# Performance work log

Hardware: AMD Instinct MI355X
Metric: run time of the kernel (lower is better)

## Reference

```python
import jax, jax.numpy as jnp
import numpy as np

B, T, IN, OUT, H, N, M = 16, 1024, 64, 64, 512, 128, 40
EPS = 1e-8


def setup_inputs() -> dict:
    key = jax.random.key(0)
    ks = jax.random.split(key, 16)
    s = 0.02  # xavier-ish init scale for weights
    inp = {
        "x": jax.random.normal(ks[0], (B, T, IN), jnp.float32),
        "h0": jnp.zeros((B, H), jnp.float32),
        "c0": jnp.zeros((B, H), jnp.float32),
        "memory0": jax.random.normal(ks[1], (B, N, M), jnp.float32) * 0.01,
        "read0": jnp.zeros((B, M), jnp.float32),
        # LSTMCell params (torch gate order: i, f, g, o)
        "W_ih": jax.random.normal(ks[2], (4 * H, IN + M), jnp.float32) * s,
        "b_ih": jnp.zeros((4 * H,), jnp.float32),
        "W_hh": jax.random.normal(ks[3], (4 * H, H), jnp.float32) * s,
        "b_hh": jnp.zeros((4 * H,), jnp.float32),
        "W_fc": jax.random.normal(ks[4], (OUT, H), jnp.float32) * s,
        "b_fc": jnp.zeros((OUT,), jnp.float32),
        "W_e": jax.random.normal(ks[5], (M, H), jnp.float32) * s,
        "b_e": jnp.zeros((M,), jnp.float32),
        "W_a": jax.random.normal(ks[6], (M, H), jnp.float32) * s,
        "b_a": jnp.zeros((M,), jnp.float32),
        "W_k": jax.random.normal(ks[7], (M, H), jnp.float32) * s,
        "b_k": jnp.zeros((M,), jnp.float32),
        "W_b": jax.random.normal(ks[8], (1, H), jnp.float32) * s,
        "b_b": jnp.zeros((1,), jnp.float32),
    }
    return inp


def _ntm_scan(x, h0, c0, memory0, read0, W_ih, b_ih, W_hh, b_hh,
              W_fc, b_fc, W_e, b_e, W_a, b_a, W_k, b_k, W_b, b_b):
    def step(carry, x_t):
        h, c, mem, r = carry
        # controller LSTM cell on [x_t, read_vector]
        inp = jnp.concatenate([x_t, r], axis=-1)            # [B, IN+M]
        gates = inp @ W_ih.T + b_ih + h @ W_hh.T + b_hh      # [B, 4H]
        i, f, g, o = jnp.split(gates, 4, axis=-1)
        i = jax.nn.sigmoid(i); f = jax.nn.sigmoid(f)
        g = jnp.tanh(g);       o = jax.nn.sigmoid(o)
        c = f * c + i * g
        h = o * jnp.tanh(c)
        out = jnp.tanh(h @ W_fc.T + b_fc)                    # [B, OUT]
        # content addressing
        key = jnp.tanh(h @ W_k.T + b_k)                      # [B, M]
        beta = jax.nn.softplus(h @ W_b.T + b_b) + EPS        # [B, 1]
        kn = key / (jnp.linalg.norm(key, axis=-1, keepdims=True) + EPS)
        mn = mem / (jnp.linalg.norm(mem, axis=-1, keepdims=True) + EPS)
        sim = jnp.einsum('bnm,bm->bn', mn, kn)               # [B, N]
        w = jax.nn.softmax(beta * sim, axis=-1)              # [B, N]
        # erase/add write, then read from updated memory
        e = jax.nn.sigmoid(h @ W_e.T + b_e)                  # [B, M]
        a = jnp.tanh(h @ W_a.T + b_a)                        # [B, M]
        mem = mem * (1.0 - w[:, :, None] * e[:, None, :]) + w[:, :, None] * a[:, None, :]
        r = jnp.einsum('bn,bnm->bm', w, mem)                 # [B, M]
        return (h, c, mem, r), out

    xs = jnp.swapaxes(x, 0, 1)                               # [T, B, IN]
    (h, c, mem, r), outs = jax.lax.scan(step, (h0, c0, memory0, read0), xs)
    return jnp.swapaxes(outs, 0, 1), h, c                    # [B, T, OUT]


def reference(x, h0, c0, memory0, read0, W_ih, b_ih, W_hh, b_hh,
              W_fc, b_fc, W_e, b_e, W_a, b_a, W_k, b_k, W_b, b_b):
    return _ntm_scan(x, h0, c0, memory0, read0, W_ih, b_ih, W_hh, b_hh,
                     W_fc, b_fc, W_e, b_e, W_a, b_a, W_k, b_k, W_b, b_b)
```

## Files before the change

### kernel.cpp

```cpp
#include <hip/hip_runtime.h>
#include <math.h>

#define Bq   16
#define Tq   1024
#define OUTq 64
#define Hq   512
#define Nq   128
#define Mq   40
#define NT   512
#define NISL 16
#define GWG  13
#define IWG  14
#define NWG  224
#define EPSq 1e-8f
#define MAGIC 0x00C0FFEEu

typedef unsigned long long ull;

__device__ __forceinline__ float sigmf(float x){ return 1.f/(1.f + expf(-x)); }
__device__ __forceinline__ float softplusf(float x){ return (x > 20.f) ? x : log1pf(expf(x)); }

__device__ __forceinline__ ull icld64(const ull* p){
  return __hip_atomic_load(p, __ATOMIC_RELAXED, __HIP_MEMORY_SCOPE_AGENT);
}
__device__ __forceinline__ void icst64(ull* p, ull v){
  __hip_atomic_store(p, v, __ATOMIC_RELAXED, __HIP_MEMORY_SCOPE_AGENT);
}
__device__ __forceinline__ ull icpoll64(const ull* p){
  ull v;
  asm volatile("global_load_dwordx2 %0, %1, off sc0 sc1\n\ts_waitcnt vmcnt(0)"
               : "=v"(v) : "v"(p) : "memory");
  return v;
}
__device__ __forceinline__ ull packtv(unsigned tag, float v){
  return ((ull)tag << 32) | (ull)__float_as_uint(v);
}
__device__ __forceinline__ float lowf(ull v){ return __uint_as_float((unsigned)v); }

__device__ __forceinline__ float waitword(const ull* sh, unsigned want, bool fast){
  if (fast){
    #pragma unroll 1
    for (int i = 0; i < 4096; ++i){
      const ull v = icpoll64(sh);
      if ((unsigned)(v >> 32) == want) return lowf(v);
      __builtin_amdgcn_s_sleep(1);
    }
  }
  #pragma unroll 1
  for (;;){
    const ull v = icld64(sh);
    if ((unsigned)(v >> 32) == want) return lowf(v);
    __builtin_amdgcn_s_sleep(1);
  }
}

__device__ __forceinline__ int ready_and_handshake(ull* rdy, ull* magic, int blk){
  __hip_atomic_fetch_add(rdy, 1ull, __ATOMIC_RELAXED, __HIP_MEMORY_SCOPE_AGENT);
  while (icld64(rdy) < (ull)NWG) __builtin_amdgcn_s_sleep(8);
  if (blk == 0) icst64(magic, ((ull)MAGIC << 32) | 1ull);
  #pragma unroll 1
  for (int i = 0; i < 4000; ++i){
    if ((unsigned)(icpoll64(magic) >> 32) == MAGIC) return 1;
    __builtin_amdgcn_s_sleep(2);
  }
  return 0;
}

extern "C" __global__ void __launch_bounds__(NT, 1)
ntm_kernel(const float* __restrict__ xg,  const float* __restrict__ h0g,
           const float* __restrict__ c0g, const float* __restrict__ mem0g,
           const float* __restrict__ read0g,
           const float* __restrict__ Wih, const float* __restrict__ bih,
           const float* __restrict__ Whh, const float* __restrict__ bhh,
           const float* __restrict__ Wfc, const float* __restrict__ bfc,
           const float* __restrict__ We,  const float* __restrict__ be,
           const float* __restrict__ Wa,  const float* __restrict__ ba,
           const float* __restrict__ Wk,  const float* __restrict__ bk,
           const float* __restrict__ Wb,  const float* __restrict__ bbeta,
           float* __restrict__ yout, ull* __restrict__ rdy,
           ull* __restrict__ h_sh, ull* __restrict__ r_sh)
{
  const int blk = blockIdx.x;
  const int tid = threadIdx.x;
  const int x   = blk & 7;
  const int j   = blk >> 3;
  const int bat = (j < IWG) ? x : (x + 8);
  const int slot= (j < IWG) ? j : (j - IWG);
  __shared__ __align__(16) char smem[41344];
  __shared__ int s_fast;
  ull* magic = rdy + 1;

  if (slot < GWG){
    float* inp_s  = (float*)smem;
    float* red_s  = (float*)(smem + 2560);
    float* rw_s   = (float*)(smem + 13440);
    float* r_s    = (float*)(smem + 39680);
    float* gate_s = (float*)(smem + 39840);
    float* c_s    = (float*)(smem + 40480);
    float* bias_s = (float*)(smem + 40640);

    const int kseg  = tid & 15;
    const int rslot = tid >> 4;
    const int nd    = (slot < 12) ? 40 : 32;
    const int d0    = slot * 40;
    const int rowsR = 4 * nd;

    float4 w4[5][9];
    #pragma unroll
    for (int rr = 0; rr < 5; ++rr){
      const int row = rslot*5 + rr;
      if (row < rowsR){
        const int gate = row / nd, ld = row - gate*nd;
        const int grow = gate*Hq + d0 + ld;
        #pragma unroll
        for (int kk = 0; kk < 9; ++kk){
          float v[4];
          #pragma unroll
          for (int c4 = 0; c4 < 4; ++c4){
            const int k = kseg*36 + kk*4 + c4;
            v[c4] = (k < 64) ? Wih[grow*104 + k] : Whh[grow*512 + (k - 64)];
          }
          w4[rr][kk] = make_float4(v[0], v[1], v[2], v[3]);
        }
      } else {
        #pragma unroll
        for (int kk = 0; kk < 9; ++kk) w4[rr][kk] = make_float4(0.f,0.f,0.f,0.f);
      }
    }
    if (tid < rowsR){
      const int gate = tid / nd, ld = tid - gate*nd;
      const int grow = gate*Hq + d0 + ld;
      bias_s[tid] = bih[grow] + bhh[grow];
    }
    for (int i = tid; i < rowsR*40; i += NT){
      const int row = i / 40, m = i - row*40;
      const int gate = row / nd, ld = row - gate*nd;
      const int grow = gate*Hq + d0 + ld;
      rw_s[row*41 + m] = Wih[grow*104 + 64 + m];
    }
    if (tid < nd) c_s[tid] = c0g[bat*Hq + d0 + tid];
    if (tid < 16)
      *(float4*)&inp_s[tid*4] = ((const float4*)xg)[(bat*Tq + 0)*16 + tid];
    if (tid < 128)
      *(float4*)&inp_s[64 + tid*4] = ((const float4*)h0g)[bat*128 + tid];
    __syncthreads();
    if (tid == 0) s_fast = ready_and_handshake(rdy, magic, blk);
    __syncthreads();
    const bool fast = (s_fast != 0);

    for (int t = 0; t < Tq; ++t){
      const int p = t & 1, pm = (t - 1) & 1;
      float acc[5] = {0.f,0.f,0.f,0.f,0.f};
      {
        const float* bp = inp_s + kseg*36;
        #pragma unroll
        for (int kk = 0; kk < 9; ++kk){
          const float4 f = *(const float4*)&bp[kk*4];
          #pragma unroll
          for (int rr = 0; rr < 5; ++rr)
            acc[rr] += w4[rr][kk].x*f.x + w4[rr][kk].y*f.y
                     + w4[rr][kk].z*f.z + w4[rr][kk].w*f.w;
        }
      }
      #pragma unroll
      for (int rr = 0; rr < 5; ++rr)
        red_s[(rslot*5 + rr)*17 + kseg] = acc[rr];
      if (t == 0){
        if (tid < 40) r_s[tid] = read0g[bat*Mq + tid];
      } else if (tid < 40){
        const int idx = (pm*NISL + bat)*Mq + tid;
        r_s[tid] = waitword(&r_sh[idx], (unsigned)t, fast);
      }
      __syncthreads();
      if (tid < rowsR){
        float s2 = bias_s[tid];
        const float* rp = &red_s[tid*17];
        #pragma unroll
        for (int q = 0; q < 16; ++q) s2 += rp[q];
        const float* rwp = &rw_s[tid*41];
        #pragma unroll
        for (int m = 0; m < 40; ++m) s2 += rwp[m]*r_s[m];
        gate_s[tid] = s2;
      }
      __syncthreads();
      if (tid < nd){
        const float gi = gate_s[tid];
        const float gf = gate_s[nd + tid];
        const float gc = gate_s[2*nd + tid];
        const float go = gate_s[3*nd + tid];
        const float iv = sigmf(gi), fv = sigmf(gf), gv = tanhf(gc), ov = sigmf(go);
        const float cn = fv*c_s[tid] + iv*gv;
        const float hn = ov*tanhf(cn);
        c_s[tid] = cn;
        const int idx = (p*NISL + bat)*Hq + d0 + tid;
        icst64(&h_sh[idx], packtv((unsigned)(t+1), hn));
        if (t == Tq - 1){
          yout[Bq*Tq*OUTq + bat*Hq + d0 + tid] = hn;
          yout[Bq*Tq*OUTq + Bq*Hq + bat*Hq + d0 + tid] = cn;
        }
      }
      {
        const int idx = (p*NISL + bat)*Hq + tid;
        inp_s[64 + tid] = waitword(&h_sh[idx], (unsigned)(t+1), fast);
      }
      if (t + 1 < Tq && tid < 16)
        *(float4*)&inp_s[tid*4] = ((const float4*)xg)[(bat*Tq + t + 1)*16 + tid];
      __syncthreads();
    }
  }
  else {
    float* mem_s  = (float*)smem;
    float* h_s    = (float*)(smem + 22528);
    float* hred_s = (float*)(smem + 24576);
    float* key_s  = (float*)(smem + 26624);
    float* e_s    = (float*)(smem + 26784);
    float* a_s    = (float*)(smem + 26944);
    float* w_s    = (float*)(smem + 27104);
    float* rred_s = (float*)(smem + 27616);
    float* ored_s = (float*)(smem + 29056);

    #pragma unroll
    for (int q = 0; q < 10; ++q){
      const int e = q*512 + tid;
      const int n = e / 40, m = e - n*40;
      mem_s[n*44 + m] = mem0g[bat*(Nq*Mq) + e];
    }
    const int o  = tid & 127;
    const int kc = tid >> 7;
    const float* wrow = (o < 40) ? (Wk + o*Hq)
                      : (o < 80) ? (We + (o-40)*Hq)
                      : (o < 120) ? (Wa + (o-80)*Hq)
                      : (o == 120) ? Wb : nullptr;
    float4 wv2[32];
    if (wrow){
      #pragma unroll
      for (int kk = 0; kk < 32; ++kk)
        wv2[kk] = *(const float4*)&wrow[kc*128 + kk*4];
    } else {
      #pragma unroll
      for (int kk = 0; kk < 32; ++kk) wv2[kk] = make_float4(0.f,0.f,0.f,0.f);
    }
    float4 wfc[16];
    {
      const int o2 = tid & 63, kc8 = tid >> 6;
      #pragma unroll
      for (int kk = 0; kk < 16; ++kk)
        wfc[kk] = *(const float4*)&Wfc[o2*Hq + kc8*64 + kk*4];
    }
    const float bfcv = bfc[tid & 63];
    float hb0 = 0.f, hb1 = 0.f;
    if (tid < 64){
      const int o0 = tid, o1 = tid + 64;
      hb0 = (o0 < 40) ? bk[o0] : be[o0-40];
      hb1 = (o1 < 80) ? be[o1-40] : (o1 < 120) ? ba[o1-80]
          : (o1 == 120) ? bbeta[0] : 0.f;
    }
    __syncthreads();
    if (tid == 0) s_fast = ready_and_handshake(rdy, magic, blk);
    __syncthreads();
    const bool fast = (s_fast != 0);

    for (int t = 0; t < Tq; ++t){
      const int p = t & 1;
      const unsigned want = (unsigned)(t + 1);
      {
        const int idx = (p*NISL + bat)*Hq + tid;
        h_s[tid] = waitword(&h_sh[idx], want, fast);
      }
      __syncthreads();
      {
        float a0 = 0.f;
        const float* hp = h_s + kc*128;
        #pragma unroll
        for (int kk = 0; kk < 32; ++kk){
          const float4 f = *(const float4*)&hp[kk*4];
          a0 += wv2[kk].x*f.x + wv2[kk].y*f.y + wv2[kk].z*f.z + wv2[kk].w*f.w;
        }
        hred_s[o*4 + kc] = a0;
      }
      __syncthreads();
      if (tid < 64){
        const int l = tid;
        const float4 p0 = *(const float4*)&hred_s[l*4];
        const float4 p1 = *(const float4*)&hred_s[(l+64)*4];
        float s0 = hb0 + p0.x + p0.y + p0.z + p0.w;
        float s1 = hb1 + p1.x + p1.y + p1.z + p1.w;
        float kv = 0.f;
        if (l < 40){ kv = tanhf(s0); key_s[l] = kv; }
        else        { e_s[l-40] = sigmf(s0); }
        if (l < 16)      e_s[l+24]  = sigmf(s1);
        else if (l < 56) a_s[l-16]  = tanhf(s1);
        float bval = softplusf(s1) + EPSq;
        const float bet = __shfl(bval, 56);
        float ss = kv*kv;
        #pragma unroll
        for (int off = 32; off; off >>= 1) ss += __shfl_xor(ss, off);
        const float rinv = 1.f/(sqrtf(ss) + EPSq);
        float sc[2];
        #pragma unroll
        for (int half = 0; half < 2; ++half){
          const int n = l + 64*half;
          float qq = 0.f, dd = 0.f;
          const float* mrow = &mem_s[n*44];
          #pragma unroll
          for (int q = 0; q < 10; ++q){
            const float4 mv = *(const float4*)&mrow[q*4];
            const float4 kvv = *(const float4*)&key_s[q*4];
            qq += mv.x*mv.x + mv.y*mv.y + mv.z*mv.z + mv.w*mv.w;
            dd += mv.x*kvv.x + mv.y*kvv.y + mv.z*kvv.z + mv.w*kvv.w;
          }
          sc[half] = bet * dd * rinv / (sqrtf(qq) + EPSq);
        }
        const float e0 = expf(sc[0]), e1 = expf(sc[1]);
        float sm = e0 + e1;
        #pragma unroll
        for (int off = 32; off; off >>= 1) sm += __shfl_xor(sm, off);
        const float inv = 1.f/sm;
        w_s[l] = e0*inv; w_s[l+64] = e1*inv;
      }
      __syncthreads();
      if (tid < 320){
        const int m = tid % 40, ng = tid / 40;
        const float ev = e_s[m], av = a_s[m];
        float part = 0.f;
        #pragma unroll
        for (int q = 0; q < 16; ++q){
          const int n = ng*16 + q, idx2 = n*44 + m;
          const float mv = mem_s[idx2];
          const float wn = w_s[n];
          const float nv = fmaf(wn, fmaf(-ev, mv, av), mv);
          mem_s[idx2] = nv;
          part = fmaf(wn, nv, part);
        }
        rred_s[m*9 + ng] = part;
      }
      __syncthreads();
      if (tid < 40){
        float r = 0.f;
        #pragma unroll
        for (int q = 0; q < 8; ++q) r += rred_s[tid*9 + q];
        const int idx = (p*NISL + bat)*Mq + tid;
        icst64(&r_sh[idx], packtv(want, r));
      }
      {
        const int o2 = tid & 63, kc8 = tid >> 6;
        float a0 = 0.f;
        const float* hp = h_s + kc8*64;
        #pragma unroll
        for (int kk = 0; kk < 16; ++kk){
          const float4 f = *(const float4*)&hp[kk*4];
          a0 += wfc[kk].x*f.x + wfc[kk].y*f.y + wfc[kk].z*f.z + wfc[kk].w*f.w;
        }
        ored_s[o2*9 + kc8] = a0;
      }
      __syncthreads();
      if (tid < 64){
        float s2 = bfcv;
        const float* op = &ored_s[tid*9];
        #pragma unroll
        for (int q = 0; q < 8; ++q) s2 += op[q];
        yout[(bat*Tq + t)*OUTq + tid] = tanhf(s2);
      }
      __syncthreads();
    }
  }
}

extern "C" void kernel_launch(void* const* d_in, const int* in_sizes, int n_in,
                              void* d_out, int out_size, void* d_ws, size_t ws_size,
                              hipStream_t stream){
  const float* xg    = (const float*)d_in[0];
  const float* h0g   = (const float*)d_in[1];
  const float* c0g   = (const float*)d_in[2];
  const float* mem0g = (const float*)d_in[3];
  const float* read0g= (const float*)d_in[4];
  const float* Wih   = (const float*)d_in[5];
  const float* bih   = (const float*)d_in[6];
  const float* Whh   = (const float*)d_in[7];
  const float* bhh   = (const float*)d_in[8];
  const float* Wfc   = (const float*)d_in[9];
  const float* bfc   = (const float*)d_in[10];
  const float* We    = (const float*)d_in[11];
  const float* be    = (const float*)d_in[12];
  const float* Wa    = (const float*)d_in[13];
  const float* ba    = (const float*)d_in[14];
  const float* Wk    = (const float*)d_in[15];
  const float* bk    = (const float*)d_in[16];
  const float* Wb    = (const float*)d_in[17];
  const float* bbeta = (const float*)d_in[18];

  float* yout  = (float*)d_out;
  ull*   rdy   = (ull*)d_ws;
  ull*   h_sh  = (ull*)((char*)d_ws + 4096);
  ull*   r_sh  = (ull*)((char*)d_ws + 135168);

  hipMemsetAsync(d_ws, 0, 147456, stream);
  hipLaunchKernelGGL(ntm_kernel, dim3(NWG), dim3(NT), 0, stream,
                     xg, h0g, c0g, mem0g, read0g, Wih, bih, Whh, bhh,
                     Wfc, bfc, We, be, Wa, ba, Wk, bk, Wb, bbeta,
                     yout, rdy, h_sh, r_sh);
}
```

Baseline: 6.419 ms.

## Offload head projections of h to gate workgroups and publish partial sums

```diff
diff --git a/kernel.cpp b/kernel.cpp
--- a/kernel.cpp
+++ b/kernel.cpp
@@ -78,7 +78,8 @@
            const float* __restrict__ Wk,  const float* __restrict__ bk,
            const float* __restrict__ Wb,  const float* __restrict__ bbeta,
            float* __restrict__ yout, ull* __restrict__ rdy,
-           ull* __restrict__ h_sh, ull* __restrict__ r_sh)
+           ull* __restrict__ h_sh, ull* __restrict__ r_sh,
+           ull* __restrict__ hp_sh)
 {
   const int blk = blockIdx.x;
   const int tid = threadIdx.x;
@@ -86,7 +87,7 @@
   const int j   = blk >> 3;
   const int bat = (j < IWG) ? x : (x + 8);
   const int slot= (j < IWG) ? j : (j - IWG);
-  __shared__ __align__(16) char smem[41344];
+  __shared__ __align__(16) char smem[61760];
   __shared__ int s_fast;
   ull* magic = rdy + 1;
 
@@ -94,10 +95,11 @@
     float* inp_s  = (float*)smem;
     float* red_s  = (float*)(smem + 2560);
     float* rw_s   = (float*)(smem + 13440);
-    float* r_s    = (float*)(smem + 39680);
-    float* gate_s = (float*)(smem + 39840);
-    float* c_s    = (float*)(smem + 40480);
-    float* bias_s = (float*)(smem + 40640);
+    float* hw_s   = (float*)(smem + 39680);
+    float* r_s    = (float*)(smem + 60160);
+    float* gate_s = (float*)(smem + 60320);
+    float* c_s    = (float*)(smem + 60960);
+    float* bias_s = (float*)(smem + 61120);
 
     const int kseg  = tid & 15;
     const int rslot = tid >> 4;
@@ -137,6 +139,17 @@
       const int gate = row / nd, ld = row - gate*nd;
       const int grow = gate*Hq + d0 + ld;
       rw_s[row*41 + m] = Wih[grow*104 + 64 + m];
+    }
+    for (int i = tid; i < 10*512; i += NT){
+      const int lr = i >> 9, d = i & 511;
+      const int grow = slot*10 + lr;
+      float v = 0.f;
+      if (grow < 121){
+        v = (grow < 40) ? Wk[grow*Hq + d]
+          : (grow < 80) ? We[(grow-40)*Hq + d]
+          : (grow < 120) ? Wa[(grow-80)*Hq + d] : Wb[d];
+      }
+      hw_s[i] = v;
     }
     if (tid < nd) c_s[tid] = c0g[bat*Hq + d0 + tid];
     if (tid < 16)
@@ -206,18 +219,37 @@
       if (t + 1 < Tq && tid < 16)
         *(float4*)&inp_s[tid*4] = ((const float4*)xg)[(bat*Tq + t + 1)*16 + tid];
       __syncthreads();
+      if (tid < 320){
+        const int grp = tid >> 5, ln = tid & 31;
+        const int grow = slot*10 + grp;
+        if (grow < 121){
+          const float* wp  = &hw_s[grp*512 + ln*16];
+          const float* hp2 = &inp_s[64 + ln*16];
+          float ps = 0.f;
+          #pragma unroll
+          for (int q = 0; q < 4; ++q){
+            const float4 wv = *(const float4*)&wp[q*4];
+            const float4 hv = *(const float4*)&hp2[q*4];
+            ps += wv.x*hv.x + wv.y*hv.y + wv.z*hv.z + wv.w*hv.w;
+          }
+          #pragma unroll
+          for (int off = 16; off; off >>= 1) ps += __shfl_xor(ps, off);
+          if (ln == 0)
+            icst64(&hp_sh[(p*NISL + bat)*128 + grow], packtv((unsigned)(t+1), ps));
+        }
+      }
     }
   }
   else {
     float* mem_s  = (float*)smem;
     float* h_s    = (float*)(smem + 22528);
     float* hred_s = (float*)(smem + 24576);
-    float* key_s  = (float*)(smem + 26624);
-    float* e_s    = (float*)(smem + 26784);
-    float* a_s    = (float*)(smem + 26944);
-    float* w_s    = (float*)(smem + 27104);
-    float* rred_s = (float*)(smem + 27616);
-    float* ored_s = (float*)(smem + 29056);
+    float* key_s  = (float*)(smem + 25088);
+    float* e_s    = (float*)(smem + 25248);
+    float* a_s    = (float*)(smem + 25408);
+    float* w_s    = (float*)(smem + 25568);
+    float* rred_s = (float*)(smem + 26080);
+    float* ored_s = (float*)(smem + 27520);
 
     #pragma unroll
     for (int q = 0; q < 10; ++q){
@@ -225,21 +257,7 @@
       const int n = e / 40, m = e - n*40;
       mem_s[n*44 + m] = mem0g[bat*(Nq*Mq) + e];
     }
-    const int o  = tid & 127;
-    const int kc = tid >> 7;
-    const float* wrow = (o < 40) ? (Wk + o*Hq)
-                      : (o < 80) ? (We + (o-40)*Hq)
-                      : (o < 120) ? (Wa + (o-80)*Hq)
-                      : (o == 120) ? Wb : nullptr;
-    float4 wv2[32];
-    if (wrow){
-      #pragma unroll
-      for (int kk = 0; kk < 32; ++kk)
-        wv2[kk] = *(const float4*)&wrow[kc*128 + kk*4];
-    } else {
-      #pragma unroll
-      for (int kk = 0; kk < 32; ++kk) wv2[kk] = make_float4(0.f,0.f,0.f,0.f);
-    }
+    if (tid < 128) hred_s[tid] = 0.f;
     float4 wfc[16];
     {
       const int o2 = tid & 63, kc8 = tid >> 6;
@@ -263,28 +281,13 @@
     for (int t = 0; t < Tq; ++t){
       const int p = t & 1;
       const unsigned want = (unsigned)(t + 1);
-      {
-        const int idx = (p*NISL + bat)*Hq + tid;
-        h_s[tid] = waitword(&h_sh[idx], want, fast);
-      }
-      __syncthreads();
-      {
-        float a0 = 0.f;
-        const float* hp = h_s + kc*128;
-        #pragma unroll
-        for (int kk = 0; kk < 32; ++kk){
-          const float4 f = *(const float4*)&hp[kk*4];
-          a0 += wv2[kk].x*f.x + wv2[kk].y*f.y + wv2[kk].z*f.z + wv2[kk].w*f.w;
-        }
-        hred_s[o*4 + kc] = a0;
-      }
+      if (tid < 121)
+        hred_s[tid] = waitword(&hp_sh[(p*NISL + bat)*128 + tid], want, fast);
       __syncthreads();
       if (tid < 64){
         const int l = tid;
-        const float4 p0 = *(const float4*)&hred_s[l*4];
-        const float4 p1 = *(const float4*)&hred_s[(l+64)*4];
-        float s0 = hb0 + p0.x + p0.y + p0.z + p0.w;
-        float s1 = hb1 + p1.x + p1.y + p1.z + p1.w;
+        float s0 = hb0 + hred_s[l];
+        float s1 = hb1 + hred_s[64 + l];
         float kv = 0.f;
         if (l < 40){ kv = tanhf(s0); key_s[l] = kv; }
         else        { e_s[l-40] = sigmf(s0); }
@@ -342,6 +345,11 @@
         const int idx = (p*NISL + bat)*Mq + tid;
         icst64(&r_sh[idx], packtv(want, r));
       }
+      {
+        const int idx = (p*NISL + bat)*Hq + tid;
+        h_s[tid] = waitword(&h_sh[idx], want, fast);
+      }
+      __syncthreads();
       {
         const int o2 = tid & 63, kc8 = tid >> 6;
         float a0 = 0.f;
@@ -393,10 +401,11 @@
   ull*   rdy   = (ull*)d_ws;
   ull*   h_sh  = (ull*)((char*)d_ws + 4096);
   ull*   r_sh  = (ull*)((char*)d_ws + 135168);
-
-  hipMemsetAsync(d_ws, 0, 147456, stream);
+  ull*   hp_sh = (ull*)((char*)d_ws + 147456);
+
+  hipMemsetAsync(d_ws, 0, 180224, stream);
   hipLaunchKernelGGL(ntm_kernel, dim3(NWG), dim3(NT), 0, stream,
                      xg, h0g, c0g, mem0g, read0g, Wih, bih, Whh, bhh,
                      Wfc, bfc, We, be, Wa, ba, Wk, bk, Wb, bbeta,
-                     yout, rdy, h_sh, r_sh);
-}
+                     yout, rdy, h_sh, r_sh, hp_sh);
+}
```

New measurement: 7.354 ms. 14.6% more time.
